# Kernel optimization log

Hardware: AMD Instinct MI355X
Metric: run time of the kernel (lower is better)

The kernel has to match this reference:

```python
import jax, jax.numpy as jnp
import numpy as np

N_NODES = 50000
N_EDGES = 800000
N_FEAT = 128
HIDDEN = 64
N_GRAPHS = 256


def setup_inputs() -> dict:
    key = jax.random.key(0)
    ks = jax.random.split(key, 10)
    x = jax.random.normal(ks[0], (N_NODES, N_FEAT), dtype=jnp.float32)
    edge_index = jax.random.randint(ks[1], (2, N_EDGES), 0, N_NODES, dtype=jnp.int64)
    batch = jnp.sort(jax.random.randint(ks[2], (N_NODES,), 0, N_GRAPHS, dtype=jnp.int64))
    s1 = 1.0 / np.sqrt(N_FEAT)
    s2 = 1.0 / np.sqrt(HIDDEN)
    W1 = jax.random.normal(ks[3], (N_FEAT, HIDDEN), dtype=jnp.float32) * s1
    b1 = jnp.zeros((HIDDEN,), dtype=jnp.float32)
    W2 = jax.random.normal(ks[4], (HIDDEN, HIDDEN), dtype=jnp.float32) * s2
    b2 = jnp.zeros((HIDDEN,), dtype=jnp.float32)
    Wm1 = jax.random.normal(ks[5], (HIDDEN, HIDDEN), dtype=jnp.float32) * s2
    bm1 = jnp.zeros((HIDDEN,), dtype=jnp.float32)
    Wm2 = jax.random.normal(ks[6], (HIDDEN, 1), dtype=jnp.float32) * s2
    bm2 = jnp.zeros((1,), dtype=jnp.float32)
    return {"x": x, "edge_index": edge_index, "batch": batch,
            "W1": W1, "b1": b1, "W2": W2, "b2": b2,
            "Wm1": Wm1, "bm1": bm1, "Wm2": Wm2, "bm2": bm2}


def _gcn_layer(h, W, b, src, dst, norm, n_nodes):
    # GCNConv: h @ W, then symmetric-normalized scatter-add over edges (+ self-loops), + bias
    h = h @ W
    msg = h[src] * norm[:, None]              # [E+N, H] gather + scale
    agg = jax.ops.segment_sum(msg, dst, num_segments=n_nodes)
    return agg + b


def reference(x, edge_index, batch, W1, b1, W2, b2, Wm1, bm1, Wm2, bm2):
    n = x.shape[0]
    loops = jnp.arange(n, dtype=edge_index.dtype)
    src = jnp.concatenate([edge_index[0], loops])  # self-loops as in PyG GCNConv
    dst = jnp.concatenate([edge_index[1], loops])
    deg = jax.ops.segment_sum(jnp.ones_like(dst, dtype=x.dtype), dst, num_segments=n)
    dis = jnp.where(deg > 0, jax.lax.rsqrt(deg), 0.0)  # deg^-1/2
    norm = dis[src] * dis[dst]

    h = jax.nn.relu(_gcn_layer(x, W1, b1, src, dst, norm, n))
    h = jax.nn.relu(_gcn_layer(h, W2, b2, src, dst, norm, n))

    # global mean pool over graphs
    sums = jax.ops.segment_sum(h, batch, num_segments=N_GRAPHS)
    cnts = jax.ops.segment_sum(jnp.ones((n,), dtype=h.dtype), batch, num_segments=N_GRAPHS)
    pooled = sums / jnp.maximum(cnts, 1.0)[:, None]

    # MLP head (dropout inactive at eval)
    out = jax.nn.relu(pooled @ Wm1 + bm1) @ Wm2 + bm2
    return out.reshape(-1)
```

## Files before the change

### kernel.cpp

```cpp
#include <hip/hip_runtime.h>

#define NN 50000
#define NE 800000
#define NF 128
#define NH 64
#define NG 256
#define NB 196
#define NC 196
#define CH 4096
#define CELL 80
#define CAP 5120
#define NGB 782

typedef __attribute__((ext_vector_type(8))) short bf16x8;
typedef __attribute__((ext_vector_type(4))) float f32x4;

static __device__ __forceinline__ unsigned short f2bf(float f) {
    union { float f; unsigned u; } v; v.f = f;
    unsigned r = v.u + 0x7FFF + ((v.u >> 16) & 1);
    return (unsigned short)(r >> 16);
}
static __device__ __forceinline__ float lo16(unsigned u) {
    return __uint_as_float(u << 16);
}
static __device__ __forceinline__ float hi16(unsigned u) {
    return __uint_as_float(u & 0xFFFF0000u);
}
static __device__ __forceinline__ unsigned pack2(float a, float b) {
    return (unsigned)f2bf(a) | ((unsigned)f2bf(b) << 16);
}

__global__ __launch_bounds__(256) void prep_gemm(const int* __restrict__ ei,
                                                 int* __restrict__ histg,
                                                 unsigned* __restrict__ ebuf,
                                                 const float* __restrict__ X,
                                                 const float* __restrict__ W,
                                                 const float* __restrict__ W2,
                                                 unsigned short* __restrict__ Y,
                                                 float* __restrict__ psum,
                                                 unsigned* __restrict__ W2p) {
    __shared__ __align__(16) char smem[35840];
    const int t = threadIdx.x;

    if (blockIdx.x < NC) {
        int* hist = (int*)smem;
        int* incl = hist + 256;
        int* lcur = incl + 256;
        int* wq   = lcur + 256;
        unsigned* lpairs = (unsigned*)(smem + 4096);
        const int c = blockIdx.x;
        const int c0 = c * CH;

        hist[t] = 0;
        __syncthreads();

        int es[16], ed[16];
#pragma unroll
        for (int j = 0; j < 4; ++j) {
            const int e = c0 + (j * 256 + t) * 4;
            int4 s4 = make_int4(-1, -1, -1, -1);
            int4 d4 = make_int4(-1, -1, -1, -1);
            if (e + 3 < NE) {
                s4 = *(const int4*)&ei[e];
                d4 = *(const int4*)&ei[NE + e];
            } else {
                if (e < NE)     { s4.x = ei[e];     d4.x = ei[NE + e]; }
                if (e + 1 < NE) { s4.y = ei[e + 1]; d4.y = ei[NE + e + 1]; }
                if (e + 2 < NE) { s4.z = ei[e + 2]; d4.z = ei[NE + e + 2]; }
            }
            es[4*j] = s4.x; es[4*j+1] = s4.y; es[4*j+2] = s4.z; es[4*j+3] = s4.w;
            ed[4*j] = d4.x; ed[4*j+1] = d4.y; ed[4*j+2] = d4.z; ed[4*j+3] = d4.w;
            if (d4.x >= 0) atomicAdd(&hist[d4.x >> 8], 1);
            if (d4.y >= 0) atomicAdd(&hist[d4.y >> 8], 1);
            if (d4.z >= 0) atomicAdd(&hist[d4.z >> 8], 1);
            if (d4.w >= 0) atomicAdd(&hist[d4.w >> 8], 1);
        }
        __syncthreads();

        const int v = hist[t];
        int sv = v;
#pragma unroll
        for (int off = 1; off < 64; off <<= 1) {
            int u = __shfl_up(sv, off, 64);
            if ((t & 63) >= off) sv += u;
        }
        if ((t & 63) == 63) wq[t >> 6] = sv;
        __syncthreads();
        {
            const int wid = t >> 6;
            int add = 0;
            if (wid > 0) add += wq[0];
            if (wid > 1) add += wq[1];
            if (wid > 2) add += wq[2];
            sv += add;
        }
        incl[t] = sv;
        lcur[t] = sv - v;
        if (t < NB) histg[c * NB + t] = v;
        __syncthreads();

#pragma unroll
        for (int j = 0; j < 16; ++j) {
            const int d = ed[j];
            if (d >= 0) {
                int p = atomicAdd(&lcur[d >> 8], 1);
                lpairs[p] = (unsigned)es[j] | ((unsigned)d << 16);
            }
        }
        __syncthreads();

        const int total = incl[255];
        for (int p = t; p < total; p += 256) {
            const unsigned pr = lpairs[p];
            const int b = pr >> 24;
            const int i = p - (incl[b] - hist[b]);
            ebuf[(b * NC + c) * CELL + i] = pr;
        }
    } else {
        const int gb = blockIdx.x - NC;
        if (gb >= NGB) {
            for (int idx = t; idx < 2048; idx += 256) {
                const int n = idx >> 5, kp = idx & 31;
                W2p[idx] = pack2(W2[(2 * kp) * 64 + n], W2[(2 * kp + 1) * 64 + n]);
            }
            return;
        }
        if (gb < 17) {
            const int o = gb * 1024 + t * 4;
            if (o < 16640) *(float4*)&psum[o] = make_float4(0.f, 0.f, 0.f, 0.f);
        }

        unsigned short* Xs = (unsigned short*)smem;
        unsigned int* Wt = (unsigned int*)(smem + 17408);
        const int base = gb * 64;

        for (int i = t * 4; i < 64 * 128; i += 1024) {
            int node = i >> 7, k = i & 127;
            int gn = base + node; if (gn >= NN) gn = NN - 1;
            float4 v = *(const float4*)&X[(size_t)gn * 128 + k];
            ushort4 o = { f2bf(v.x), f2bf(v.y), f2bf(v.z), f2bf(v.w) };
            *(ushort4*)&Xs[node * 136 + k] = o;
        }
        for (int idx = t; idx < 64 * 64; idx += 256) {
            int n = idx & 63, kp = idx >> 6;
            float w0 = W[(2 * kp) * 64 + n];
            float w1 = W[(2 * kp + 1) * 64 + n];
            Wt[n * 68 + kp] = (unsigned)f2bf(w0) | ((unsigned)f2bf(w1) << 16);
        }
        __syncthreads();

        const int w = t >> 6;
        const int lane = t & 63;
        const int l15 = lane & 15;
        const int quad = lane >> 4;
        f32x4 acc[4] = {{0.f,0.f,0.f,0.f},{0.f,0.f,0.f,0.f},{0.f,0.f,0.f,0.f},{0.f,0.f,0.f,0.f}};
#pragma unroll
        for (int kk = 0; kk < 4; ++kk) {
            const bf16x8 a = *(const bf16x8*)&Xs[(w * 16 + l15) * 136 + quad * 8 + kk * 32];
#pragma unroll
            for (int nt = 0; nt < 4; ++nt) {
                const bf16x8 b = *(const bf16x8*)&Wt[(nt * 16 + l15) * 68 + quad * 4 + kk * 16];
                acc[nt] = __builtin_amdgcn_mfma_f32_16x16x32_bf16(a, b, acc[nt], 0, 0, 0);
            }
        }
        const int r0 = base + w * 16 + quad * 4;
#pragma unroll
        for (int reg = 0; reg < 4; ++reg) {
            const int row = r0 + reg;
            if (row < NN) {
#pragma unroll
                for (int nt = 0; nt < 4; ++nt)
                    Y[(size_t)row * 64 + nt * 16 + l15] = f2bf(acc[nt][reg]);
            }
        }
    }
}

__global__ __launch_bounds__(512) void build_csr(const unsigned* __restrict__ ebuf,
                                                 const int* __restrict__ histg,
                                                 int2* __restrict__ row_range,
                                                 float* __restrict__ dis,
                                                 int* __restrict__ csr_src) {
    const int b = blockIdx.x, t = threadIdx.x;
    const int e0 = b * CAP;
    __shared__ int coffs[256];
    __shared__ int cvs[256];
    __shared__ int deg_l[256];
    __shared__ int pre[256];
    __shared__ int cur[256];
    __shared__ int wq[8];
    __shared__ unsigned lpairs[CAP];
    __shared__ int lsrc[CAP];

    int cv = 0;
    if (t < NC) cv = histg[t * NB + b];
    int sv = cv;
    if (t < 256) {
#pragma unroll
        for (int off = 1; off < 64; off <<= 1) {
            int u = __shfl_up(sv, off, 64);
            if ((t & 63) >= off) sv += u;
        }
        if ((t & 63) == 63) wq[t >> 6] = sv;
        deg_l[t] = (b * 256 + t < NN) ? 1 : 0;
        cvs[t] = cv;
    }
    __syncthreads();
    if (t < 256) {
        const int wid = t >> 6;
        int add = 0;
        if (wid > 0) add += wq[0];
        if (wid > 1) add += wq[1];
        if (wid > 2) add += wq[2];
        coffs[t] = sv + add;
    }
    __syncthreads();

    {
        const int tc = t & 255;
        const int cv2 = cvs[tc];
        if (tc < NC && cv2 > 0) {
            const uint4* src4 = (const uint4*)&ebuf[(size_t)(b * NC + tc) * CELL];
            const int dst = coffs[tc] - cv2;
            for (int g4 = (t >> 8); g4 * 4 < cv2; g4 += 2) {
                const uint4 u = src4[g4];
                const int i = g4 * 4;
                lpairs[dst + i] = u.x;
                if (i + 1 < cv2) lpairs[dst + i + 1] = u.y;
                if (i + 2 < cv2) lpairs[dst + i + 2] = u.z;
                if (i + 3 < cv2) lpairs[dst + i + 3] = u.w;
            }
        }
    }
    __syncthreads();

    const int total = coffs[255];
    for (int i = t; i < total; i += 512)
        atomicAdd(&deg_l[(lpairs[i] >> 16) & 255], 1);
    __syncthreads();

    int dvi = 0, psv = 0;
    if (t < 256) {
        dvi = deg_l[t];
        psv = dvi;
#pragma unroll
        for (int off = 1; off < 64; off <<= 1) {
            int u = __shfl_up(psv, off, 64);
            if ((t & 63) >= off) psv += u;
        }
        if ((t & 63) == 63) wq[4 + (t >> 6)] = psv;
    }
    __syncthreads();
    if (t < 256) {
        const int wid = t >> 6;
        int add = 0;
        if (wid > 0) add += wq[4];
        if (wid > 1) add += wq[5];
        if (wid > 2) add += wq[6];
        psv += add;
        pre[t] = psv;
        cur[t] = 1;
        const int nd = b * 256 + t;
        if (nd < NN) {
            const int excl = psv - dvi;
            lsrc[excl] = nd;
            row_range[nd] = make_int2(e0 + excl, e0 + psv);
            dis[nd] = rsqrtf((float)dvi);
        }
    }
    __syncthreads();

    for (int i = t; i < total; i += 512) {
        const unsigned p = lpairs[i];
        const int d = (p >> 16) & 255;
        const int pos = (pre[d] - deg_l[d]) + atomicAdd(&cur[d], 1);
        lsrc[pos] = (int)(p & 0xFFFFu);
    }
    __syncthreads();
    const int tot_all = pre[255];
    for (int i = t; i < tot_all; i += 512)
        csr_src[e0 + i] = lsrc[i];
}

static __device__ __forceinline__ void acc8(float* acc, const uint4 u) {
    acc[0] += lo16(u.x); acc[1] += hi16(u.x);
    acc[2] += lo16(u.y); acc[3] += hi16(u.y);
    acc[4] += lo16(u.z); acc[5] += hi16(u.z);
    acc[6] += lo16(u.w); acc[7] += hi16(u.w);
}
static __device__ __forceinline__ void fma8(float* acc, const uint4 u, const float d) {
    acc[0] = fmaf(lo16(u.x), d, acc[0]); acc[1] = fmaf(hi16(u.x), d, acc[1]);
    acc[2] = fmaf(lo16(u.y), d, acc[2]); acc[3] = fmaf(hi16(u.y), d, acc[3]);
    acc[4] = fmaf(lo16(u.z), d, acc[4]); acc[5] = fmaf(hi16(u.z), d, acc[5]);
    acc[6] = fmaf(lo16(u.w), d, acc[6]); acc[7] = fmaf(hi16(u.w), d, acc[7]);
}

static __device__ __forceinline__ void gather_rows(const unsigned short* __restrict__ h,
                                                   const int* __restrict__ csr,
                                                   int lo, int hi, int p8, float* acc) {
    int i = lo;
    for (; i + 8 <= hi; i += 8) {
        int idx[8];
#pragma unroll
        for (int j = 0; j < 8; ++j) idx[j] = csr[i + j];
        uint4 u[8];
#pragma unroll
        for (int j = 0; j < 8; ++j) u[j] = *(const uint4*)&h[(idx[j] << 6) + p8];
#pragma unroll
        for (int j = 0; j < 8; ++j) acc8(acc, u[j]);
    }
    if (i + 4 <= hi) {
        int idx[4];
#pragma unroll
        for (int j = 0; j < 4; ++j) idx[j] = csr[i + j];
        uint4 u[4];
#pragma unroll
        for (int j = 0; j < 4; ++j) u[j] = *(const uint4*)&h[(idx[j] << 6) + p8];
#pragma unroll
        for (int j = 0; j < 4; ++j) acc8(acc, u[j]);
        i += 4;
    }
    if (i + 2 <= hi) {
        const int i0 = csr[i], i1 = csr[i + 1];
        const uint4 u0 = *(const uint4*)&h[(i0 << 6) + p8];
        const uint4 u1 = *(const uint4*)&h[(i1 << 6) + p8];
        acc8(acc, u0); acc8(acc, u1);
        i += 2;
    }
    if (i < hi) acc8(acc, *(const uint4*)&h[(csr[i] << 6) + p8]);
}

static __device__ __forceinline__ void gather_rows_scaled(const unsigned short* __restrict__ h,
                                                          const int* __restrict__ csr,
                                                          const float* __restrict__ dis,
                                                          int lo, int hi, int p8, float* acc) {
    int i = lo;
    for (; i + 8 <= hi; i += 8) {
        int idx[8];
#pragma unroll
        for (int j = 0; j < 8; ++j) idx[j] = csr[i + j];
        float d[8];
#pragma unroll
        for (int j = 0; j < 8; ++j) d[j] = dis[idx[j]];
        uint4 u[8];
#pragma unroll
        for (int j = 0; j < 8; ++j) u[j] = *(const uint4*)&h[(idx[j] << 6) + p8];
#pragma unroll
        for (int j = 0; j < 8; ++j) fma8(acc, u[j], d[j]);
    }
    if (i + 4 <= hi) {
        int idx[4];
#pragma unroll
        for (int j = 0; j < 4; ++j) idx[j] = csr[i + j];
        float d[4];
#pragma unroll
        for (int j = 0; j < 4; ++j) d[j] = dis[idx[j]];
        uint4 u[4];
#pragma unroll
        for (int j = 0; j < 4; ++j) u[j] = *(const uint4*)&h[(idx[j] << 6) + p8];
#pragma unroll
        for (int j = 0; j < 4; ++j) fma8(acc, u[j], d[j]);
        i += 4;
    }
    if (i + 2 <= hi) {
        const int i0 = csr[i], i1 = csr[i + 1];
        const float d0 = dis[i0], d1 = dis[i1];
        const uint4 u0 = *(const uint4*)&h[(i0 << 6) + p8];
        const uint4 u1 = *(const uint4*)&h[(i1 << 6) + p8];
        fma8(acc, u0, d0); fma8(acc, u1, d1);
        i += 2;
    }
    if (i < hi) {
        const int i0 = csr[i];
        fma8(acc, *(const uint4*)&h[(i0 << 6) + p8], dis[i0]);
    }
}

__global__ __launch_bounds__(256) void agg_gemv(const unsigned short* __restrict__ h,
                                                const int2* __restrict__ row_range,
                                                const int* __restrict__ csr_src,
                                                const float* __restrict__ dis,
                                                const float* __restrict__ b1,
                                                const unsigned* __restrict__ W2p,
                                                unsigned short* __restrict__ g) {
    __shared__ unsigned short W2b[64 * 72];
    __shared__ unsigned short A[32 * 72];
    const int t = threadIdx.x;
    const int base = blockIdx.x * 32;
    const int nloc = t >> 3;
    const int p8 = (t & 7) * 8;
    const int n = base + nloc;
    float acc[8] = {};
    if (n < NN) {
        const int2 rr = row_range[n];
        gather_rows_scaled(h, csr_src, dis, rr.x, rr.y, p8, acc);
        const float dn = dis[n];
        const float4 bv0 = *(const float4*)&b1[p8];
        const float4 bv1 = *(const float4*)&b1[p8 + 4];
        acc[0] = fmaxf(acc[0] * dn + bv0.x, 0.f);
        acc[1] = fmaxf(acc[1] * dn + bv0.y, 0.f);
        acc[2] = fmaxf(acc[2] * dn + bv0.z, 0.f);
        acc[3] = fmaxf(acc[3] * dn + bv0.w, 0.f);
        acc[4] = fmaxf(acc[4] * dn + bv1.x, 0.f);
        acc[5] = fmaxf(acc[5] * dn + bv1.y, 0.f);
        acc[6] = fmaxf(acc[6] * dn + bv1.z, 0.f);
        acc[7] = fmaxf(acc[7] * dn + bv1.w, 0.f);
    }
    for (int idx = t; idx < 2048; idx += 256) {
        const int nn2 = idx >> 5, kp = idx & 31;
        *(unsigned*)&W2b[nn2 * 72 + 2 * kp] = W2p[idx];
    }
    uint4 pk;
    pk.x = pack2(acc[0], acc[1]);
    pk.y = pack2(acc[2], acc[3]);
    pk.z = pack2(acc[4], acc[5]);
    pk.w = pack2(acc[6], acc[7]);
    *(uint4*)&A[nloc * 72 + p8] = pk;
    __syncthreads();

    const int w = t >> 6;
    const int lane = t & 63;
    const int l15 = lane & 15;
    const int quad = lane >> 4;
    const int mt = w & 1;
    const int nq = (w >> 1) * 2;
    const bf16x8 a0 = *(const bf16x8*)&A[(mt * 16 + l15) * 72 + quad * 8];
    const bf16x8 a1 = *(const bf16x8*)&A[(mt * 16 + l15) * 72 + 32 + quad * 8];
    const bf16x8 b00 = *(const bf16x8*)&W2b[(nq * 16 + l15) * 72 + quad * 8];
    const bf16x8 b01 = *(const bf16x8*)&W2b[(nq * 16 + l15) * 72 + 32 + quad * 8];
    const bf16x8 b10 = *(const bf16x8*)&W2b[((nq + 1) * 16 + l15) * 72 + quad * 8];
    const bf16x8 b11 = *(const bf16x8*)&W2b[((nq + 1) * 16 + l15) * 72 + 32 + quad * 8];
    f32x4 c0 = {0.f, 0.f, 0.f, 0.f}, c1 = {0.f, 0.f, 0.f, 0.f};
    c0 = __builtin_amdgcn_mfma_f32_16x16x32_bf16(a0, b00, c0, 0, 0, 0);
    c0 = __builtin_amdgcn_mfma_f32_16x16x32_bf16(a1, b01, c0, 0, 0, 0);
    c1 = __builtin_amdgcn_mfma_f32_16x16x32_bf16(a0, b10, c1, 0, 0, 0);
    c1 = __builtin_amdgcn_mfma_f32_16x16x32_bf16(a1, b11, c1, 0, 0, 0);
    const int r0 = base + mt * 16 + quad * 4;
    float4 d4 = *(const float4*)&dis[r0];
    const float dd[4] = { d4.x, d4.y, d4.z, d4.w };
#pragma unroll
    for (int reg = 0; reg < 4; ++reg) {
        const int row = r0 + reg;
        if (row < NN) {
            g[(size_t)row * 64 + nq * 16 + l15] = f2bf(c0[reg] * dd[reg]);
            g[(size_t)row * 64 + (nq + 1) * 16 + l15] = f2bf(c1[reg] * dd[reg]);
        }
    }
}

__global__ __launch_bounds__(256) void agg_pool(const unsigned short* __restrict__ h,
                                                const int2* __restrict__ row_range,
                                                const int* __restrict__ csr_src,
                                                const float* __restrict__ dis,
                                                const float* __restrict__ bias,
                                                const int* __restrict__ batch,
                                                float* __restrict__ psum,
                                                float* __restrict__ cnt) {
    __shared__ float rowsL[32 * 68];
    __shared__ int nb[32];
    const int t = threadIdx.x;
    const int nloc = t >> 3;
    const int n = blockIdx.x * 32 + nloc;
    const int p8 = (t & 7) * 8;
    if ((t & 7) == 0) nb[nloc] = (n < NN) ? batch[n] : -1;
    if (n < NN) {
        const int2 rr = row_range[n];
        float acc[8] = {};
        gather_rows(h, csr_src, rr.x, rr.y, p8, acc);
        const float dn = dis[n];
        const float4 bv0 = *(const float4*)&bias[p8];
        const float4 bv1 = *(const float4*)&bias[p8 + 4];
        float4 r0, r1;
        r0.x = fmaxf(acc[0] * dn + bv0.x, 0.f);
        r0.y = fmaxf(acc[1] * dn + bv0.y, 0.f);
        r0.z = fmaxf(acc[2] * dn + bv0.z, 0.f);
        r0.w = fmaxf(acc[3] * dn + bv0.w, 0.f);
        r1.x = fmaxf(acc[4] * dn + bv1.x, 0.f);
        r1.y = fmaxf(acc[5] * dn + bv1.y, 0.f);
        r1.z = fmaxf(acc[6] * dn + bv1.z, 0.f);
        r1.w = fmaxf(acc[7] * dn + bv1.w, 0.f);
        *(float4*)&rowsL[nloc * 68 + p8] = r0;
        *(float4*)&rowsL[nloc * 68 + p8 + 4] = r1;
    }
    __syncthreads();
    if (t < 64) {
        float s = 0.f; int curg = -2; int rl = 0;
        for (int r = 0; r < 32; ++r) {
            const int gg = nb[r];
            if (gg != curg) {
                if (curg >= 0) {
                    atomicAdd(&psum[curg * 64 + t], s);
                    if (t == 0) atomicAdd(&cnt[curg], (float)rl);
                }
                s = 0.f; rl = 0; curg = gg;
            }
            if (gg >= 0) { s += rowsL[r * 68 + t]; ++rl; }
        }
        if (curg >= 0) {
            atomicAdd(&psum[curg * 64 + t], s);
            if (t == 0) atomicAdd(&cnt[curg], (float)rl);
        }
    }
}

__global__ __launch_bounds__(64) void head_kernel(const float* __restrict__ psum,
                                                  const float* __restrict__ cnt,
                                                  const float* __restrict__ Wm1,
                                                  const float* __restrict__ bm1,
                                                  const float* __restrict__ Wm2,
                                                  const float* __restrict__ bm2,
                                                  float* __restrict__ out) {
    const int g = blockIdx.x;
    const int t = threadIdx.x;
    __shared__ float pl[64];
    const float inv = 1.f / fmaxf(cnt[g], 1.f);
    pl[t] = psum[g * 64 + t] * inv;
    __syncthreads();
    float z = bm1[t];
#pragma unroll 8
    for (int k = 0; k < 64; ++k)
        z += pl[k] * Wm1[k * 64 + t];
    z = fmaxf(z, 0.f);
    float y = z * Wm2[t];
    for (int off = 32; off; off >>= 1) y += __shfl_down(y, off);
    if (t == 0) out[g] = y + bm2[0];
}

extern "C" void kernel_launch(void* const* d_in, const int* in_sizes, int n_in,
                              void* d_out, int out_size, void* d_ws, size_t ws_size,
                              hipStream_t stream) {
    const float* x   = (const float*)d_in[0];
    const int*   ei  = (const int*)d_in[1];
    const int*   bat = (const int*)d_in[2];
    const float* W1  = (const float*)d_in[3];
    const float* b1  = (const float*)d_in[4];
    const float* W2  = (const float*)d_in[5];
    const float* b2  = (const float*)d_in[6];
    const float* Wm1 = (const float*)d_in[7];
    const float* bm1 = (const float*)d_in[8];
    const float* Wm2 = (const float*)d_in[9];
    const float* bm2 = (const float*)d_in[10];
    float* out = (float*)d_out;

    char* w = (char*)d_ws;
    int*            histg     = (int*)           (w + 0);
    int2*           row_range = (int2*)          (w + 153664);
    float*          dis       = (float*)         (w + 553664);
    int*            csr_src   = (int*)           (w + 753664);
    unsigned*       ebuf      = (unsigned*)      (w + 4767744);
    unsigned short* bufA      = (unsigned short*)(w + 17060864);
    unsigned short* bufB      = (unsigned short*)(w + 23460864);
    float*          psum      = (float*)         (w + 29860864);
    unsigned*       W2p       = (unsigned*)      (w + 29927424);
    float*          cnt       = psum + 16384;

    prep_gemm <<<NC + NGB + 1, 256, 0, stream>>>(ei, histg, ebuf, x, W1, W2, bufA, psum, W2p);
    build_csr <<<NB, 512, 0, stream>>>(ebuf, histg, row_range, dis, csr_src);
    agg_gemv  <<<(NN + 31) / 32, 256, 0, stream>>>(bufA, row_range, csr_src, dis, b1, W2p, bufB);
    agg_pool  <<<(NN + 31) / 32, 256, 0, stream>>>(bufB, row_range, csr_src, dis, b2, bat, psum, cnt);
    head_kernel<<<NG, 64, 0, stream>>>(psum, cnt, Wm1, bm1, Wm2, bm2, out);
}
```

Baseline: 149.2 us.

## Split feature dims into two planar halves for cache-friendly gathers, separate second GEMM

Hidden features are now stored as two planes of 32 bf16 columns, and each aggregation pass is launched over both halves as separate block ranges. The aim is to halve the gathered working set per block so random row gathers hit L2 more often. The fused aggregate+GEMV kernel is split into agg1, a standalone gemm2 over 64-node tiles, and agg2_pool. This adds an extra kernel launch and an extra intermediate buffer round trip through memory. The pooling atomics are also issued separately per half.

New measurement: 163.9 us. 9.8% more time.

```diff
diff --git a/kernel.cpp b/kernel.cpp
--- a/kernel.cpp
+++ b/kernel.cpp
@@ -11,6 +11,8 @@
 #define CELL 80
 #define CAP 5120
 #define NGB 782
+#define NPB 782
+#define PS (NN * 32)
 
 typedef __attribute__((ext_vector_type(8))) short bf16x8;
 typedef __attribute__((ext_vector_type(4))) float f32x4;
@@ -169,8 +171,10 @@
             const int row = r0 + reg;
             if (row < NN) {
 #pragma unroll
-                for (int nt = 0; nt < 4; ++nt)
-                    Y[(size_t)row * 64 + nt * 16 + l15] = f2bf(acc[nt][reg]);
+                for (int nt = 0; nt < 4; ++nt) {
+                    const int p = nt >> 1;
+                    Y[(size_t)p * PS + row * 32 + (nt & 1) * 16 + l15] = f2bf(acc[nt][reg]);
+                }
             }
         }
     }
@@ -295,9 +299,9 @@
     acc[6] = fmaf(lo16(u.w), d, acc[6]); acc[7] = fmaf(hi16(u.w), d, acc[7]);
 }
 
-static __device__ __forceinline__ void gather_rows(const unsigned short* __restrict__ h,
-                                                   const int* __restrict__ csr,
-                                                   int lo, int hi, int p8, float* acc) {
+static __device__ __forceinline__ void gatherP(const unsigned short* __restrict__ h,
+                                               const int* __restrict__ csr,
+                                               int lo, int hi, int off8, float* acc) {
     int i = lo;
     for (; i + 8 <= hi; i += 8) {
         int idx[8];
@@ -305,7 +309,7 @@
         for (int j = 0; j < 8; ++j) idx[j] = csr[i + j];
         uint4 u[8];
 #pragma unroll
-        for (int j = 0; j < 8; ++j) u[j] = *(const uint4*)&h[(idx[j] << 6) + p8];
+        for (int j = 0; j < 8; ++j) u[j] = *(const uint4*)&h[(idx[j] << 5) + off8];
 #pragma unroll
         for (int j = 0; j < 8; ++j) acc8(acc, u[j]);
     }
@@ -315,25 +319,25 @@
         for (int j = 0; j < 4; ++j) idx[j] = csr[i + j];
         uint4 u[4];
 #pragma unroll
-        for (int j = 0; j < 4; ++j) u[j] = *(const uint4*)&h[(idx[j] << 6) + p8];
+        for (int j = 0; j < 4; ++j) u[j] = *(const uint4*)&h[(idx[j] << 5) + off8];
 #pragma unroll
         for (int j = 0; j < 4; ++j) acc8(acc, u[j]);
         i += 4;
     }
     if (i + 2 <= hi) {
         const int i0 = csr[i], i1 = csr[i + 1];
-        const uint4 u0 = *(const uint4*)&h[(i0 << 6) + p8];
-        const uint4 u1 = *(const uint4*)&h[(i1 << 6) + p8];
+        const uint4 u0 = *(const uint4*)&h[(i0 << 5) + off8];
+        const uint4 u1 = *(const uint4*)&h[(i1 << 5) + off8];
         acc8(acc, u0); acc8(acc, u1);
         i += 2;
     }
-    if (i < hi) acc8(acc, *(const uint4*)&h[(csr[i] << 6) + p8]);
-}
-
-static __device__ __forceinline__ void gather_rows_scaled(const unsigned short* __restrict__ h,
-                                                          const int* __restrict__ csr,
-                                                          const float* __restrict__ dis,
-                                                          int lo, int hi, int p8, float* acc) {
+    if (i < hi) acc8(acc, *(const uint4*)&h[(csr[i] << 5) + off8]);
+}
+
+static __device__ __forceinline__ void gatherP_scaled(const unsigned short* __restrict__ h,
+                                                      const int* __restrict__ csr,
+                                                      const float* __restrict__ dis,
+                                                      int lo, int hi, int off8, float* acc) {
     int i = lo;
     for (; i + 8 <= hi; i += 8) {
         int idx[8];
@@ -344,7 +348,7 @@
         for (int j = 0; j < 8; ++j) d[j] = dis[idx[j]];
         uint4 u[8];
 #pragma unroll
-        for (int j = 0; j < 8; ++j) u[j] = *(const uint4*)&h[(idx[j] << 6) + p8];
+        for (int j = 0; j < 8; ++j) u[j] = *(const uint4*)&h[(idx[j] << 5) + off8];
 #pragma unroll
         for (int j = 0; j < 8; ++j) fma8(acc, u[j], d[j]);
     }
@@ -357,7 +361,7 @@
         for (int j = 0; j < 4; ++j) d[j] = dis[idx[j]];
         uint4 u[4];
 #pragma unroll
-        for (int j = 0; j < 4; ++j) u[j] = *(const uint4*)&h[(idx[j] << 6) + p8];
+        for (int j = 0; j < 4; ++j) u[j] = *(const uint4*)&h[(idx[j] << 5) + off8];
 #pragma unroll
         for (int j = 0; j < 4; ++j) fma8(acc, u[j], d[j]);
         i += 4;
@@ -365,111 +369,126 @@
     if (i + 2 <= hi) {
         const int i0 = csr[i], i1 = csr[i + 1];
         const float d0 = dis[i0], d1 = dis[i1];
-        const uint4 u0 = *(const uint4*)&h[(i0 << 6) + p8];
-        const uint4 u1 = *(const uint4*)&h[(i1 << 6) + p8];
+        const uint4 u0 = *(const uint4*)&h[(i0 << 5) + off8];
+        const uint4 u1 = *(const uint4*)&h[(i1 << 5) + off8];
         fma8(acc, u0, d0); fma8(acc, u1, d1);
         i += 2;
     }
     if (i < hi) {
         const int i0 = csr[i];
-        fma8(acc, *(const uint4*)&h[(i0 << 6) + p8], dis[i0]);
-    }
-}
-
-__global__ __launch_bounds__(256) void agg_gemv(const unsigned short* __restrict__ h,
-                                                const int2* __restrict__ row_range,
-                                                const int* __restrict__ csr_src,
-                                                const float* __restrict__ dis,
-                                                const float* __restrict__ b1,
-                                                const unsigned* __restrict__ W2p,
-                                                unsigned short* __restrict__ g) {
-    __shared__ unsigned short W2b[64 * 72];
-    __shared__ unsigned short A[32 * 72];
+        fma8(acc, *(const uint4*)&h[(i0 << 5) + off8], dis[i0]);
+    }
+}
+
+__global__ __launch_bounds__(256) void agg1(const unsigned short* __restrict__ h,
+                                            const int2* __restrict__ row_range,
+                                            const int* __restrict__ csr_src,
+                                            const float* __restrict__ dis,
+                                            const float* __restrict__ b1,
+                                            unsigned short* __restrict__ bufH) {
     const int t = threadIdx.x;
-    const int base = blockIdx.x * 32;
-    const int nloc = t >> 3;
-    const int p8 = (t & 7) * 8;
-    const int n = base + nloc;
+    const int half = (blockIdx.x >= NPB) ? 1 : 0;
+    const int gb = blockIdx.x - half * NPB;
+    const int nloc = t >> 2;
+    const int off8 = (t & 3) * 8;
+    const int n = gb * 64 + nloc;
+    if (n >= NN) return;
+    const unsigned short* hp = h + (size_t)half * PS;
+    const int2 rr = row_range[n];
     float acc[8] = {};
-    if (n < NN) {
-        const int2 rr = row_range[n];
-        gather_rows_scaled(h, csr_src, dis, rr.x, rr.y, p8, acc);
-        const float dn = dis[n];
-        const float4 bv0 = *(const float4*)&b1[p8];
-        const float4 bv1 = *(const float4*)&b1[p8 + 4];
-        acc[0] = fmaxf(acc[0] * dn + bv0.x, 0.f);
-        acc[1] = fmaxf(acc[1] * dn + bv0.y, 0.f);
-        acc[2] = fmaxf(acc[2] * dn + bv0.z, 0.f);
-        acc[3] = fmaxf(acc[3] * dn + bv0.w, 0.f);
-        acc[4] = fmaxf(acc[4] * dn + bv1.x, 0.f);
-        acc[5] = fmaxf(acc[5] * dn + bv1.y, 0.f);
-        acc[6] = fmaxf(acc[6] * dn + bv1.z, 0.f);
-        acc[7] = fmaxf(acc[7] * dn + bv1.w, 0.f);
-    }
-    for (int idx = t; idx < 2048; idx += 256) {
-        const int nn2 = idx >> 5, kp = idx & 31;
-        *(unsigned*)&W2b[nn2 * 72 + 2 * kp] = W2p[idx];
-    }
+    gatherP_scaled(hp, csr_src, dis, rr.x, rr.y, off8, acc);
+    const float dn = dis[n];
+    const float4 bv0 = *(const float4*)&b1[half * 32 + off8];
+    const float4 bv1 = *(const float4*)&b1[half * 32 + off8 + 4];
+    acc[0] = fmaxf(acc[0] * dn + bv0.x, 0.f);
+    acc[1] = fmaxf(acc[1] * dn + bv0.y, 0.f);
+    acc[2] = fmaxf(acc[2] * dn + bv0.z, 0.f);
+    acc[3] = fmaxf(acc[3] * dn + bv0.w, 0.f);
+    acc[4] = fmaxf(acc[4] * dn + bv1.x, 0.f);
+    acc[5] = fmaxf(acc[5] * dn + bv1.y, 0.f);
+    acc[6] = fmaxf(acc[6] * dn + bv1.z, 0.f);
+    acc[7] = fmaxf(acc[7] * dn + bv1.w, 0.f);
     uint4 pk;
     pk.x = pack2(acc[0], acc[1]);
     pk.y = pack2(acc[2], acc[3]);
     pk.z = pack2(acc[4], acc[5]);
     pk.w = pack2(acc[6], acc[7]);
-    *(uint4*)&A[nloc * 72 + p8] = pk;
+    *(uint4*)&bufH[(size_t)n * 64 + half * 32 + off8] = pk;
+}
+
+__global__ __launch_bounds__(256) void gemm2(const unsigned short* __restrict__ bufH,
+                                             const unsigned* __restrict__ W2p,
+                                             const float* __restrict__ dis,
+                                             unsigned short* __restrict__ bufB) {
+    __shared__ unsigned short Ah[64 * 72];
+    __shared__ unsigned short W2b[64 * 72];
+    const int t = threadIdx.x;
+    const int base = blockIdx.x * 64;
+    for (int i = t * 8; i < 64 * 64; i += 2048) {
+        const int node = i >> 6, k = i & 63;
+        *(uint4*)&Ah[node * 72 + k] = *(const uint4*)&bufH[(size_t)(base + node) * 64 + k];
+    }
+    for (int idx = t; idx < 2048; idx += 256) {
+        const int nn2 = idx >> 5, kp = idx & 31;
+        *(unsigned*)&W2b[nn2 * 72 + 2 * kp] = W2p[idx];
+    }
     __syncthreads();
 
     const int w = t >> 6;
     const int lane = t & 63;
     const int l15 = lane & 15;
     const int quad = lane >> 4;
-    const int mt = w & 1;
-    const int nq = (w >> 1) * 2;
-    const bf16x8 a0 = *(const bf16x8*)&A[(mt * 16 + l15) * 72 + quad * 8];
-    const bf16x8 a1 = *(const bf16x8*)&A[(mt * 16 + l15) * 72 + 32 + quad * 8];
-    const bf16x8 b00 = *(const bf16x8*)&W2b[(nq * 16 + l15) * 72 + quad * 8];
-    const bf16x8 b01 = *(const bf16x8*)&W2b[(nq * 16 + l15) * 72 + 32 + quad * 8];
-    const bf16x8 b10 = *(const bf16x8*)&W2b[((nq + 1) * 16 + l15) * 72 + quad * 8];
-    const bf16x8 b11 = *(const bf16x8*)&W2b[((nq + 1) * 16 + l15) * 72 + 32 + quad * 8];
-    f32x4 c0 = {0.f, 0.f, 0.f, 0.f}, c1 = {0.f, 0.f, 0.f, 0.f};
-    c0 = __builtin_amdgcn_mfma_f32_16x16x32_bf16(a0, b00, c0, 0, 0, 0);
-    c0 = __builtin_amdgcn_mfma_f32_16x16x32_bf16(a1, b01, c0, 0, 0, 0);
-    c1 = __builtin_amdgcn_mfma_f32_16x16x32_bf16(a0, b10, c1, 0, 0, 0);
-    c1 = __builtin_amdgcn_mfma_f32_16x16x32_bf16(a1, b11, c1, 0, 0, 0);
-    const int r0 = base + mt * 16 + quad * 4;
+    f32x4 acc[4] = {{0.f,0.f,0.f,0.f},{0.f,0.f,0.f,0.f},{0.f,0.f,0.f,0.f},{0.f,0.f,0.f,0.f}};
+#pragma unroll
+    for (int kk = 0; kk < 2; ++kk) {
+        const bf16x8 a = *(const bf16x8*)&Ah[(w * 16 + l15) * 72 + quad * 8 + kk * 32];
+#pragma unroll
+        for (int nt = 0; nt < 4; ++nt) {
+            const bf16x8 b = *(const bf16x8*)&W2b[(nt * 16 + l15) * 72 + quad * 8 + kk * 32];
+            acc[nt] = __builtin_amdgcn_mfma_f32_16x16x32_bf16(a, b, acc[nt], 0, 0, 0);
+        }
+    }
+    const int r0 = base + w * 16 + quad * 4;
     float4 d4 = *(const float4*)&dis[r0];
     const float dd[4] = { d4.x, d4.y, d4.z, d4.w };
 #pragma unroll
     for (int reg = 0; reg < 4; ++reg) {
         const int row = r0 + reg;
         if (row < NN) {
-            g[(size_t)row * 64 + nq * 16 + l15] = f2bf(c0[reg] * dd[reg]);
-            g[(size_t)row * 64 + (nq + 1) * 16 + l15] = f2bf(c1[reg] * dd[reg]);
-        }
-    }
-}
-
-__global__ __launch_bounds__(256) void agg_pool(const unsigned short* __restrict__ h,
-                                                const int2* __restrict__ row_range,
-                                                const int* __restrict__ csr_src,
-                                                const float* __restrict__ dis,
-                                                const float* __restrict__ bias,
-                                                const int* __restrict__ batch,
-                                                float* __restrict__ psum,
-                                                float* __restrict__ cnt) {
-    __shared__ float rowsL[32 * 68];
-    __shared__ int nb[32];
+#pragma unroll
+            for (int nt = 0; nt < 4; ++nt) {
+                const int p = nt >> 1;
+                bufB[(size_t)p * PS + row * 32 + (nt & 1) * 16 + l15] = f2bf(acc[nt][reg] * dd[reg]);
+            }
+        }
+    }
+}
+
+__global__ __launch_bounds__(256) void agg2_pool(const unsigned short* __restrict__ h,
+                                                 const int2* __restrict__ row_range,
+                                                 const int* __restrict__ csr_src,
+                                                 const float* __restrict__ dis,
+                                                 const float* __restrict__ b2,
+                                                 const int* __restrict__ batch,
+                                                 float* __restrict__ psum,
+                                                 float* __restrict__ cnt) {
+    __shared__ float rowsL[64 * 36];
+    __shared__ int nb[64];
     const int t = threadIdx.x;
-    const int nloc = t >> 3;
-    const int n = blockIdx.x * 32 + nloc;
-    const int p8 = (t & 7) * 8;
-    if ((t & 7) == 0) nb[nloc] = (n < NN) ? batch[n] : -1;
+    const int half = (blockIdx.x >= NPB) ? 1 : 0;
+    const int gb = blockIdx.x - half * NPB;
+    const int nloc = t >> 2;
+    const int off8 = (t & 3) * 8;
+    const int n = gb * 64 + nloc;
+    if ((t & 3) == 0) nb[nloc] = (n < NN) ? batch[n] : -1;
     if (n < NN) {
+        const unsigned short* hp = h + (size_t)half * PS;
         const int2 rr = row_range[n];
         float acc[8] = {};
-        gather_rows(h, csr_src, rr.x, rr.y, p8, acc);
+        gatherP(hp, csr_src, rr.x, rr.y, off8, acc);
         const float dn = dis[n];
-        const float4 bv0 = *(const float4*)&bias[p8];
-        const float4 bv1 = *(const float4*)&bias[p8 + 4];
+        const float4 bv0 = *(const float4*)&b2[half * 32 + off8];
+        const float4 bv1 = *(const float4*)&b2[half * 32 + off8 + 4];
         float4 r0, r1;
         r0.x = fmaxf(acc[0] * dn + bv0.x, 0.f);
         r0.y = fmaxf(acc[1] * dn + bv0.y, 0.f);
@@ -479,26 +498,26 @@
         r1.y = fmaxf(acc[5] * dn + bv1.y, 0.f);
         r1.z = fmaxf(acc[6] * dn + bv1.z, 0.f);
         r1.w = fmaxf(acc[7] * dn + bv1.w, 0.f);
-        *(float4*)&rowsL[nloc * 68 + p8] = r0;
-        *(float4*)&rowsL[nloc * 68 + p8 + 4] = r1;
-    }
-    __syncthreads();
-    if (t < 64) {
+        *(float4*)&rowsL[nloc * 36 + off8] = r0;
+        *(float4*)&rowsL[nloc * 36 + off8 + 4] = r1;
+    }
+    __syncthreads();
+    if (t < 32) {
         float s = 0.f; int curg = -2; int rl = 0;
-        for (int r = 0; r < 32; ++r) {
+        for (int r = 0; r < 64; ++r) {
             const int gg = nb[r];
             if (gg != curg) {
                 if (curg >= 0) {
-                    atomicAdd(&psum[curg * 64 + t], s);
-                    if (t == 0) atomicAdd(&cnt[curg], (float)rl);
+                    atomicAdd(&psum[curg * 64 + half * 32 + t], s);
+                    if (t == 0 && half == 0) atomicAdd(&cnt[curg], (float)rl);
                 }
                 s = 0.f; rl = 0; curg = gg;
             }
-            if (gg >= 0) { s += rowsL[r * 68 + t]; ++rl; }
+            if (gg >= 0) { s += rowsL[r * 36 + t]; ++rl; }
         }
         if (curg >= 0) {
-            atomicAdd(&psum[curg * 64 + t], s);
-            if (t == 0) atomicAdd(&cnt[curg], (float)rl);
+            atomicAdd(&psum[curg * 64 + half * 32 + t], s);
+            if (t == 0 && half == 0) atomicAdd(&cnt[curg], (float)rl);
         }
     }
 }
@@ -549,14 +568,16 @@
     int*            csr_src   = (int*)           (w + 753664);
     unsigned*       ebuf      = (unsigned*)      (w + 4767744);
     unsigned short* bufA      = (unsigned short*)(w + 17060864);
-    unsigned short* bufB      = (unsigned short*)(w + 23460864);
-    float*          psum      = (float*)         (w + 29860864);
-    unsigned*       W2p       = (unsigned*)      (w + 29927424);
+    unsigned short* bufH      = (unsigned short*)(w + 23460864);
+    unsigned short* bufB      = (unsigned short*)(w + 29883392);
+    float*          psum      = (float*)         (w + 36283392);
+    unsigned*       W2p       = (unsigned*)      (w + 36349952);
     float*          cnt       = psum + 16384;
 
     prep_gemm <<<NC + NGB + 1, 256, 0, stream>>>(ei, histg, ebuf, x, W1, W2, bufA, psum, W2p);
     build_csr <<<NB, 512, 0, stream>>>(ebuf, histg, row_range, dis, csr_src);
-    agg_gemv  <<<(NN + 31) / 32, 256, 0, stream>>>(bufA, row_range, csr_src, dis, b1, W2p, bufB);
-    agg_pool  <<<(NN + 31) / 32, 256, 0, stream>>>(bufB, row_range, csr_src, dis, b2, bat, psum, cnt);
+    agg1      <<<2 * NPB, 256, 0, stream>>>(bufA, row_range, csr_src, dis, b1, bufH);
+    gemm2     <<<NGB, 256, 0, stream>>>(bufH, W2p, dis, bufB);
+    agg2_pool <<<2 * NPB, 256, 0, stream>>>(bufB, row_range, csr_src, dis, b2, bat, psum, cnt);
     head_kernel<<<NG, 64, 0, stream>>>(psum, cnt, Wm1, bm1, Wm2, bm2, out);
 }
```
